# Performance work log

Hardware: AMD Instinct MI355X
Metric: run time of the kernel (lower is better)

Reference implementation:

```python
import jax, jax.numpy as jnp
import numpy as np

B, N, D = 1, 2048, 2048
H, DH, DR, MP = 16, 128, 64, 4
LOCAL = H * DH // MP  # per-shard qkv width
ATTN_MASK_VALUE = -1e10
LN_EPS = 1e-5


def setup_inputs() -> dict:
    key = jax.random.key(0)
    ks = jax.random.split(key, 5)
    s = 0.02
    return {
        "x": jax.random.normal(ks[0], (B, N, D), jnp.float32),
        "ln_scale": jnp.ones((D,), jnp.float32),
        "ln_offset": jnp.zeros((D,), jnp.float32),
        "w_qkv": jax.random.normal(ks[1], (D, 3 * H * DH), jnp.float32) * s,
        "w_attn_out": jax.random.normal(ks[2], (H * DH, D), jnp.float32) * s,
        "w_ff_in": jax.random.normal(ks[3], (D, 4 * D), jnp.float32) * s,
        "b_ff_in": jnp.zeros((4 * D,), jnp.float32),
        "w_ff_out": jax.random.normal(ks[4], (4 * D, D), jnp.float32) * s,
        "b_ff_out": jnp.zeros((D,), jnp.float32),
    }


def _rotate_every_two(x):
    # (..., d) -> interleaved (-x2, x1) pairs, GPT-J style
    x1 = x[..., ::2]
    x2 = x[..., 1::2]
    return jnp.stack((-x2, x1), axis=-1).reshape(x.shape)


def _fixed_pos_embedding(n, dim):
    inv_freq = 1.0 / (10000.0 ** (np.arange(0, dim, 2, dtype=np.float32) / dim))
    ang = np.einsum("i,j->ij", np.arange(n, dtype=np.float32), inv_freq)  # [n, dim/2]
    return jnp.asarray(np.sin(ang), jnp.float32), jnp.asarray(np.cos(ang), jnp.float32)


def _apply_rotary(x, sin, cos):
    # x: [b, n, h, d_rot]; sin/cos: [n, d_rot/2] repeated pairwise -> [1, n, 1, d_rot]
    sin = jnp.repeat(sin, 2, axis=-1)[None, :, None, :]
    cos = jnp.repeat(cos, 2, axis=-1)[None, :, None, :]
    return x * cos + _rotate_every_two(x) * sin


def reference(x, ln_scale, ln_offset, w_qkv, w_attn_out, w_ff_in, b_ff_in, w_ff_out, b_ff_out):
    # ---- LayerNorm (shared input to parallel attn + FFN) ----
    mu = jnp.mean(x, axis=-1, keepdims=True)
    var = jnp.var(x, axis=-1, keepdims=True)
    h = (x - mu) * jax.lax.rsqrt(var + LN_EPS) * ln_scale + ln_offset

    # ---- Causal self-attention with partial rotary ----
    qkv = (h @ w_qkv).reshape(B, N, MP, 3 * LOCAL)  # mp-sharded layout
    q, v, k = jnp.split(qkv, [LOCAL, 2 * LOCAL], axis=-1)
    heads = lambda t: t.reshape(B, N, H, DH)  # shard_heads: [b,n,mp,local] -> [b,n,h,dh]
    q, v, k = heads(q), heads(v), heads(k)

    sin, cos = _fixed_pos_embedding(N, DR)
    q = jnp.concatenate([_apply_rotary(q[..., :DR], sin, cos), q[..., DR:]], axis=-1)
    k = jnp.concatenate([_apply_rotary(k[..., :DR], sin, cos), k[..., DR:]], axis=-1)

    attn_scale = np.float32(np.sqrt(DH))
    logits = jnp.einsum("bihd,bjhd->bhij", q, k) / attn_scale
    causal_mask = jnp.triu(jnp.ones((N, N), dtype=bool), 1)
    logits = jnp.where(causal_mask, ATTN_MASK_VALUE, logits)
    attn_w = jax.nn.softmax(logits, axis=-1)
    attn_vec = jnp.einsum("bhij,bjhd->bihd", attn_w, v).reshape(B, N, H * DH)
    attn_out = attn_vec @ w_attn_out

    # ---- FFN (parallel branch, same LN input) ----
    ff_out = jax.nn.gelu(h @ w_ff_in + b_ff_in) @ w_ff_out + b_ff_out

    return attn_out + ff_out
```

## Files before the change

### kernel.cpp

```cpp
#include <hip/hip_runtime.h>
#include <hip/hip_bf16.h>

using bf16_t = __hip_bfloat16;
typedef __attribute__((ext_vector_type(8))) __bf16 bfrag;
typedef __attribute__((ext_vector_type(4))) float f32x4;

#define MFMA16(a, b, c) __builtin_amdgcn_mfma_f32_16x16x32_bf16((a), (b), (c), 0, 0, 0)

__device__ __forceinline__ void gload_lds16(const void* g, void* l) {
  __builtin_amdgcn_global_load_lds((const __attribute__((address_space(1))) void*)g,
                                   (__attribute__((address_space(3))) void*)l, 16, 0, 0);
}

__device__ __forceinline__ float bf2f(unsigned u) { return __uint_as_float(u << 16); }

__global__ __launch_bounds__(256) void transpose_cvt4(
    const float* __restrict__ in0, bf16_t* __restrict__ out0,
    const float* __restrict__ in1, bf16_t* __restrict__ out1,
    const float* __restrict__ in2, bf16_t* __restrict__ out2,
    const float* __restrict__ in3, bf16_t* __restrict__ out3) {
  __shared__ float t[64][65];
  int b = blockIdx.x;
  const float* in; bf16_t* out; int K, N, nx;
  if (b < 3072)      { in = in0; out = out0; K = 2048; N = 6144; nx = 96; }
  else if (b < 4096) { in = in1; out = out1; K = 2048; N = 2048; nx = 32; b -= 3072; }
  else if (b < 8192) { in = in2; out = out2; K = 2048; N = 8192; nx = 128; b -= 4096; }
  else               { in = in3; out = out3; K = 8192; N = 2048; nx = 32; b -= 8192; }
  const int n0 = (b % nx) * 64, k0 = (b / nx) * 64;
  const int tx = threadIdx.x & 15, ty = threadIdx.x >> 4;
#pragma unroll
  for (int i = 0; i < 4; ++i) {
    float4 v = *(const float4*)&in[(size_t)(k0 + i * 16 + ty) * N + n0 + tx * 4];
    t[i * 16 + ty][tx * 4 + 0] = v.x; t[i * 16 + ty][tx * 4 + 1] = v.y;
    t[i * 16 + ty][tx * 4 + 2] = v.z; t[i * 16 + ty][tx * 4 + 3] = v.w;
  }
  __syncthreads();
#pragma unroll
  for (int i = 0; i < 4; ++i) {
    const int n = i * 16 + ty;
    bf16_t w[4];
#pragma unroll
    for (int j = 0; j < 4; ++j) w[j] = bf16_t(t[tx * 4 + j][n]);
    *(uint2*)&out[(size_t)(n0 + n) * K + k0 + tx * 4] = *(const uint2*)w;
  }
}

__global__ __launch_bounds__(256) void ln_kernel(const float* __restrict__ x,
    const float* __restrict__ sc, const float* __restrict__ of, bf16_t* __restrict__ h) {
  __shared__ float red[8];
  const int n = blockIdx.x, tid = threadIdx.x;
  const float* xr = x + (size_t)n * 2048;
  float4 a = ((const float4*)xr)[tid * 2];
  float4 b = ((const float4*)xr)[tid * 2 + 1];
  float s = a.x + a.y + a.z + a.w + b.x + b.y + b.z + b.w;
  float q = a.x * a.x + a.y * a.y + a.z * a.z + a.w * a.w +
            b.x * b.x + b.y * b.y + b.z * b.z + b.w * b.w;
#pragma unroll
  for (int m = 32; m; m >>= 1) { s += __shfl_xor(s, m); q += __shfl_xor(q, m); }
  if ((tid & 63) == 0) { red[(tid >> 6) * 2] = s; red[(tid >> 6) * 2 + 1] = q; }
  __syncthreads();
  s = red[0] + red[2] + red[4] + red[6];
  q = red[1] + red[3] + red[5] + red[7];
  const float mu = s * (1.f / 2048.f);
  const float inv = rsqrtf(q * (1.f / 2048.f) - mu * mu + 1e-5f);
  const int base = tid * 8;
  float v[8] = {a.x, a.y, a.z, a.w, b.x, b.y, b.z, b.w};
  bf16_t* hr = h + (size_t)n * 2048 + base;
#pragma unroll
  for (int j = 0; j < 8; ++j) hr[j] = bf16_t((v[j] - mu) * inv * sc[base + j] + of[base + j]);
}

template <int EPI>
__global__ __launch_bounds__(512, 2) void gemm8p(
    const bf16_t* __restrict__ A, int lda, const bf16_t* __restrict__ BT, int ldb,
    const float* __restrict__ bias, float* __restrict__ Cf, bf16_t* __restrict__ Cb,
    int M, int N, int K, size_t splitStride) {
  extern __shared__ __align__(16) char lds[];
  const int tid = threadIdx.x, wid = tid >> 6, lane = tid & 63;
  const int lc = lane & 15, lg = lane >> 4;
  const int bm = blockIdx.y * 256, bn = blockIdx.x * 256;
  const int wr = wid >> 2, wc = wid & 3;
  const int NT = K >> 6, niter = NT >> 1;
  const int srow = tid >> 3;
  const int scol = (((tid & 7) ^ ((tid >> 3) & 7)) << 3);
  const bf16_t* Abase = A + (size_t)blockIdx.z * K + (size_t)(bm + srow) * lda + scol;
  const bf16_t* Bbase = BT + (size_t)blockIdx.z * K + (size_t)(bn + srow) * ldb + scol;
  auto SA = [&](int T, int h) {
    char* dst = lds + (T & 1) * 32768 + h * 16384 + wid * 1024;
    const bf16_t* src = Abase + (size_t)(h * 128) * lda + T * 64;
    gload_lds16(src, dst); gload_lds16(src + (size_t)64 * lda, dst + 8192);
  };
  auto SB = [&](int T, int h) {
    char* dst = lds + 65536 + (T & 1) * 32768 + h * 16384 + wid * 1024;
    const bf16_t* src = Bbase + (size_t)(h * 128) * ldb + T * 64;
    gload_lds16(src, dst); gload_lds16(src + (size_t)64 * ldb, dst + 8192);
  };
#define FRA(d, row, kk) (*(const bfrag*)(lds + (d) * 32768 + wr * 16384 + (row) * 128 + \
    ((((kk) * 4 + lg) ^ ((row) & 7)) << 4)))
#define FRB(d, row, kk) (*(const bfrag*)(lds + 65536 + (d) * 32768 + (wc >> 1) * 16384 + \
    (row) * 128 + ((((kk) * 4 + lg) ^ ((row) & 7)) << 4)))
#define PHASE_SYNC() do { __builtin_amdgcn_s_barrier(); \
    asm volatile("s_waitcnt lgkmcnt(0)" ::: "memory"); \
    __builtin_amdgcn_sched_barrier(0); __builtin_amdgcn_s_setprio(1); } while (0)
#define PHASE_END() do { __builtin_amdgcn_s_setprio(0); __builtin_amdgcn_s_barrier(); } while (0)
#define PHASE_END_VM(lastf) do { __builtin_amdgcn_s_setprio(0); \
    if (lastf) asm volatile("s_waitcnt vmcnt(0)" ::: "memory"); \
    else       asm volatile("s_waitcnt vmcnt(4)" ::: "memory"); \
    __builtin_amdgcn_s_barrier(); } while (0)

  SB(0, 0); SB(0, 1); SA(0, 0); SA(0, 1); SB(1, 0); SB(1, 1);
  asm volatile("s_waitcnt vmcnt(4)" ::: "memory");
  __builtin_amdgcn_s_barrier();

  f32x4 acc[8][4] = {};
  const int brl = (wc & 1) * 64 + lc;

  for (int k = 0; k < niter; ++k) {
    const int T1 = 2 * k + 1, T2 = 2 * k + 2, T3 = 2 * k + 3;
    const bool last = (k == niter - 1);
    bfrag aq[4][2], b01[2][2], b23[2][2];
#pragma unroll 1
    for (int d = 0; d < 2; ++d) {
#pragma unroll
      for (int m = 0; m < 4; ++m)
#pragma unroll
        for (int kk = 0; kk < 2; ++kk) aq[m][kk] = FRA(d, m * 16 + lc, kk);
#pragma unroll
      for (int n = 0; n < 2; ++n)
#pragma unroll
        for (int kk = 0; kk < 2; ++kk) b01[n][kk] = FRB(d, brl + n * 16, kk);
      if (d == 0) SA(T1, 0); else if (!last) SA(T2, 0);
      PHASE_SYNC();
#pragma unroll
      for (int kk = 0; kk < 2; ++kk)
#pragma unroll
        for (int m = 0; m < 4; ++m) {
          acc[m][0] = MFMA16(aq[m][kk], b01[0][kk], acc[m][0]);
          acc[m][1] = MFMA16(aq[m][kk], b01[1][kk], acc[m][1]);
        }
      PHASE_END();
#pragma unroll
      for (int n = 0; n < 2; ++n)
#pragma unroll
        for (int kk = 0; kk < 2; ++kk) b23[n][kk] = FRB(d, brl + (n + 2) * 16, kk);
      if (d == 0) SA(T1, 1); else if (!last) SA(T2, 1);
      PHASE_SYNC();
#pragma unroll
      for (int kk = 0; kk < 2; ++kk)
#pragma unroll
        for (int m = 0; m < 4; ++m) {
          acc[m][2] = MFMA16(aq[m][kk], b23[0][kk], acc[m][2]);
          acc[m][3] = MFMA16(aq[m][kk], b23[1][kk], acc[m][3]);
        }
      PHASE_END();
#pragma unroll
      for (int m = 0; m < 4; ++m)
#pragma unroll
        for (int kk = 0; kk < 2; ++kk) aq[m][kk] = FRA(d, (m + 4) * 16 + lc, kk);
      if (!last) { if (d == 0) SB(T2, 0); else SB(T3, 0); }
      PHASE_SYNC();
#pragma unroll
      for (int kk = 0; kk < 2; ++kk)
#pragma unroll
        for (int m = 0; m < 4; ++m) {
          acc[4 + m][2] = MFMA16(aq[m][kk], b23[0][kk], acc[4 + m][2]);
          acc[4 + m][3] = MFMA16(aq[m][kk], b23[1][kk], acc[4 + m][3]);
        }
      PHASE_END();
      if (!last) { if (d == 0) SB(T2, 1); else SB(T3, 1); }
      PHASE_SYNC();
#pragma unroll
      for (int kk = 0; kk < 2; ++kk)
#pragma unroll
        for (int m = 0; m < 4; ++m) {
          acc[4 + m][0] = MFMA16(aq[m][kk], b01[0][kk], acc[4 + m][0]);
          acc[4 + m][1] = MFMA16(aq[m][kk], b01[1][kk], acc[4 + m][1]);
        }
      PHASE_END_VM(last);
    }
  }
#undef FRA
#undef FRB
#undef PHASE_SYNC
#undef PHASE_END
#undef PHASE_END_VM
  char* W = lds + wid * 16384;
  if (EPI & 8) {
    bf16_t* Wb = (bf16_t*)W;
    bf16_t* Cbz = Cb + (size_t)blockIdx.z * splitStride;
#pragma unroll
    for (int mc = 0; mc < 2; ++mc) {
#pragma unroll
      for (int m4 = 0; m4 < 4; ++m4) {
#pragma unroll
        for (int n = 0; n < 4; ++n) {
          const int col = bn + wc * 64 + n * 16 + lc;
          float bv = (EPI & 1) ? bias[col] : 0.f;
#pragma unroll
          for (int i = 0; i < 4; ++i) {
            float v = acc[mc * 4 + m4][n][i];
            if (EPI & 1) v += bv;
            if (EPI & 2) v = 0.5f * v * (1.f + tanhf(0.7978845608028654f * (v + 0.044715f * v * v * v)));
            Wb[(m4 * 16 + lg * 4 + i) * 72 + n * 16 + lc] = bf16_t(v);
          }
        }
      }
      asm volatile("s_waitcnt lgkmcnt(0)" ::: "memory");
      __builtin_amdgcn_sched_barrier(0);
#pragma unroll
      for (int p = 0; p < 8; ++p) {
        const int rl = p * 8 + (lane >> 3), j = lane & 7;
        uint4 v = *(const uint4*)&Wb[rl * 72 + j * 8];
        const int grow = bm + wr * 128 + mc * 64 + rl;
        const int gcol = bn + wc * 64 + j * 8;
        *(uint4*)&Cbz[(size_t)grow * N + gcol] = v;
      }
      asm volatile("s_waitcnt lgkmcnt(0)" ::: "memory");
      __builtin_amdgcn_sched_barrier(0);
    }
  } else {
    float* Wf = (float*)W;
    float* Cfz = Cf + (size_t)blockIdx.z * splitStride;
#pragma unroll
    for (int mc = 0; mc < 4; ++mc) {
#pragma unroll
      for (int m2 = 0; m2 < 2; ++m2) {
#pragma unroll
        for (int n = 0; n < 4; ++n) {
          const int col = bn + wc * 64 + n * 16 + lc;
          float bv = (EPI & 1) ? bias[col] : 0.f;
#pragma unroll
          for (int i = 0; i < 4; ++i) {
            float v = acc[mc * 2 + m2][n][i];
            if (EPI & 1) v += bv;
            if (EPI & 2) v = 0.5f * v * (1.f + tanhf(0.7978845608028654f * (v + 0.044715f * v * v * v)));
            Wf[(m2 * 16 + lg * 4 + i) * 72 + n * 16 + lc] = v;
          }
        }
      }
      asm volatile("s_waitcnt lgkmcnt(0)" ::: "memory");
      __builtin_amdgcn_sched_barrier(0);
#pragma unroll
      for (int p = 0; p < 8; ++p) {
        const int rl = p * 4 + (lane >> 4), j = lane & 15;
        float4 v = *(const float4*)&Wf[rl * 72 + j * 4];
        const int grow = bm + wr * 128 + mc * 32 + rl;
        const int gcol = bn + wc * 64 + j * 4;
        *(float4*)&Cfz[(size_t)grow * N + gcol] = v;
      }
      asm volatile("s_waitcnt lgkmcnt(0)" ::: "memory");
      __builtin_amdgcn_sched_barrier(0);
    }
  }
}

template <int NP, bool ADDIN, bool BIAS>
__global__ __launch_bounds__(256) void reduceP(const float* __restrict__ p0,
    const float* __restrict__ p1, const float* __restrict__ p2,
    const float* __restrict__ p3, const float* __restrict__ bias,
    float* __restrict__ out, int total, int colmask) {
  const int i = (blockIdx.x * 256 + threadIdx.x) * 4;
  if (i >= total) return;
  float4 v = *(const float4*)(p0 + i);
  float4 w = *(const float4*)(p1 + i);
  v.x += w.x; v.y += w.y; v.z += w.z; v.w += w.w;
  if (NP == 4) {
    float4 u = *(const float4*)(p2 + i);
    float4 z = *(const float4*)(p3 + i);
    v.x += u.x + z.x; v.y += u.y + z.y; v.z += u.z + z.z; v.w += u.w + z.w;
  }
  if (BIAS) {
    float4 b = *(const float4*)(bias + (i & colmask));
    v.x += b.x; v.y += b.y; v.z += b.z; v.w += b.w;
  }
  if (ADDIN) {
    float4 o = *(const float4*)(out + i);
    v.x += o.x; v.y += o.y; v.z += o.z; v.w += o.w;
  }
  *(float4*)(out + i) = v;
}

__global__ __launch_bounds__(256) void reduce4b(const bf16_t* __restrict__ p0,
    const bf16_t* __restrict__ p1, const bf16_t* __restrict__ p2,
    const bf16_t* __restrict__ p3, float* __restrict__ out, int total) {
  const int i = (blockIdx.x * 256 + threadIdx.x) * 8;
  if (i >= total) return;
  uint4 a0 = *(const uint4*)(p0 + i);
  uint4 a1 = *(const uint4*)(p1 + i);
  uint4 a2 = *(const uint4*)(p2 + i);
  uint4 a3 = *(const uint4*)(p3 + i);
  const unsigned* u0 = (const unsigned*)&a0;
  const unsigned* u1 = (const unsigned*)&a1;
  const unsigned* u2 = (const unsigned*)&a2;
  const unsigned* u3 = (const unsigned*)&a3;
  float r[8];
#pragma unroll
  for (int j = 0; j < 8; ++j) {
    const int w = j >> 1, sh = (j & 1) * 16;
    r[j] = bf2f((u0[w] >> sh) & 0xffffu) + bf2f((u1[w] >> sh) & 0xffffu) +
           bf2f((u2[w] >> sh) & 0xffffu) + bf2f((u3[w] >> sh) & 0xffffu);
  }
  *(float4*)(out + i) = make_float4(r[0], r[1], r[2], r[3]);
  *(float4*)(out + i + 4) = make_float4(r[4], r[5], r[6], r[7]);
}

__global__ __launch_bounds__(128) void rope_kernel(const bf16_t* __restrict__ qkv,
    bf16_t* __restrict__ qh, bf16_t* __restrict__ kh, bf16_t* __restrict__ vT) {
  const int n = blockIdx.x, hh = blockIdx.y;
  const int d = threadIdx.x;
  const int mp = hh >> 2, hi = hh & 3;
  const bf16_t* row = qkv + (size_t)n * 6144 + mp * 1536 + hi * 128;
  float q = __bfloat162float(row[d]);
  float k = __bfloat162float(row[1024 + d]);
  if (d < 64) {
    const float ang = (float)n * powf(10000.f, -(float)(d & ~1) / 64.f);
    const float sn = sinf(ang), cs = cosf(ang);
    const float qp = __shfl_xor(q, 1), kp = __shfl_xor(k, 1);
    if (d & 1) { q = q * cs + qp * sn; k = k * cs + kp * sn; }
    else       { q = q * cs - qp * sn; k = k * cs - kp * sn; }
  }
  qh[((size_t)hh * 2048 + n) * 128 + d] = bf16_t(q * 0.08838834764831845f);
  kh[((size_t)hh * 2048 + n) * 128 + d] = bf16_t(k);
  vT[((size_t)hh * 128 + d) * 2048 + n] = row[512 + d];
}

__global__ __launch_bounds__(256) void attn_kernel(const bf16_t* __restrict__ qh,
    const bf16_t* __restrict__ kh, const bf16_t* __restrict__ vT,
    bf16_t* __restrict__ Op, float2* __restrict__ ml) {
  __shared__ alignas(16) char Kbuf[2][16384];
  __shared__ alignas(16) char Vbuf[2][16384];
  __shared__ alignas(16) bf16_t Ps[4][16 * 72];
  const int p = blockIdx.x, h = blockIdx.y, z = blockIdx.z;
  const int tid = threadIdx.x, wid = tid >> 6, lane = tid & 63;
  const int lc = lane & 15, lg = lane >> 4;
  const int krow = wid * 4 + (lane >> 4);
  const int vrow = wid * 8 + (lane >> 3);

  auto stage = [&](int kv0, int d) {
#pragma unroll
    for (int i = 0; i < 4; ++i) {
      const int kr = i * 16 + krow;
      const int kch = (lane & 15) ^ (kr & 15);
      gload_lds16(kh + ((size_t)h * 2048 + kv0 + kr) * 128 + kch * 8,
                  Kbuf[d] + i * 4096 + wid * 1024);
      const int vr = i * 32 + vrow;
      const int vch = (lane & 7) ^ (vr & 7);
      gload_lds16(vT + ((size_t)h * 128 + vr) * 2048 + kv0 + vch * 8,
                  Vbuf[d] + i * 4096 + wid * 1024);
    }
  };
#define FRK(d, row, ch) (*(const bfrag*)(Kbuf[d] + (row) * 256 + (((ch) ^ ((row) & 15)) << 4)))
#define FRV(d, row, ch) (*(const bfrag*)(Vbuf[d] + (row) * 128 + (((ch) ^ ((row) & 7)) << 4)))

#pragma unroll 1
  for (int half = 0; half < 2; ++half) {
    const int qt = half ? (31 - p) : p;
    const int nkv = qt + 1;
    const int lo = (z * nkv) / 3, hi = ((z + 1) * nkv) / 3;
    const int nj = hi - lo;
    const int qr = qt * 64 + wid * 16;
    const bf16_t* Qb = qh + ((size_t)h * 2048 + qr) * 128;
    bfrag qf[4];
#pragma unroll
    for (int ks = 0; ks < 4; ++ks)
      qf[ks] = *(const bfrag*)&Qb[lc * 128 + ks * 32 + lg * 8];
    f32x4 O[8] = {};
    float mr[4] = {-1e30f, -1e30f, -1e30f, -1e30f};
    float lsum[4] = {0.f, 0.f, 0.f, 0.f};

    if (nj > 0) {
      stage(lo * 64, 0);
      asm volatile("s_waitcnt vmcnt(0)" ::: "memory");
      __builtin_amdgcn_s_barrier();
    }
#pragma unroll 1
    for (int j = 0; j < nj; ++j) {
      const int kt = lo + j, d = j & 1;
      const int kv0 = kt * 64;
      if (j + 1 < nj) stage(kv0 + 64, d ^ 1);
      f32x4 s[4];
#pragma unroll
      for (int c = 0; c < 4; ++c) {
        f32x4 a = {};
#pragma unroll
        for (int ks = 0; ks < 4; ++ks) {
          bfrag kf = FRK(d, c * 16 + lc, ks * 4 + lg);
          a = MFMA16(qf[ks], kf, a);
        }
        s[c] = a;
      }
      if (kt == qt) {
#pragma unroll
        for (int c = 0; c < 4; ++c)
#pragma unroll
          for (int i = 0; i < 4; ++i)
            if (kv0 + c * 16 + lc > qr + lg * 4 + i) s[c][i] = -1e10f;
      }
      float pm[4];
#pragma unroll
      for (int i = 0; i < 4; ++i)
        pm[i] = fmaxf(fmaxf(s[0][i], s[1][i]), fmaxf(s[2][i], s[3][i]));
#pragma unroll
      for (int m = 1; m < 16; m <<= 1)
#pragma unroll
        for (int i = 0; i < 4; ++i) pm[i] = fmaxf(pm[i], __shfl_xor(pm[i], m));
      bool small = true;
#pragma unroll
      for (int i = 0; i < 4; ++i) small = small && (pm[i] <= mr[i] + 8.f);
      const bool skip = __all(small);
      float al[4], rs[4];
#pragma unroll
      for (int i = 0; i < 4; ++i) {
        const float mn = skip ? mr[i] : fmaxf(mr[i], pm[i]);
        al[i] = __expf(mr[i] - mn);
        mr[i] = mn;
        rs[i] = 0.f;
      }
#pragma unroll
      for (int c = 0; c < 4; ++c)
#pragma unroll
        for (int i = 0; i < 4; ++i) {
          const float pv = __expf(s[c][i] - mr[i]);
          s[c][i] = pv; rs[i] += pv;
        }
#pragma unroll
      for (int m = 1; m < 16; m <<= 1)
#pragma unroll
        for (int i = 0; i < 4; ++i) rs[i] += __shfl_xor(rs[i], m);
#pragma unroll
      for (int i = 0; i < 4; ++i) lsum[i] = lsum[i] * al[i] + rs[i];
      if (!skip) {
#pragma unroll
        for (int n = 0; n < 8; ++n)
#pragma unroll
          for (int i = 0; i < 4; ++i) O[n][i] *= al[i];
      }
#pragma unroll
      for (int c = 0; c < 4; ++c)
#pragma unroll
        for (int i = 0; i < 4; ++i)
          Ps[wid][(lg * 4 + i) * 72 + c * 16 + lc] = bf16_t(s[c][i]);
#pragma unroll
      for (int k2 = 0; k2 < 2; ++k2) {
        bfrag pf = *(const bfrag*)((const char*)&Ps[wid][0] + lc * 144 + k2 * 64 + lg * 16);
#pragma unroll
        for (int n = 0; n < 8; ++n) {
          bfrag vf = FRV(d, n * 16 + lc, k2 * 4 + lg);
          O[n] = MFMA16(pf, vf, O[n]);
        }
      }
      if (j + 1 < nj) asm volatile("s_waitcnt vmcnt(0)" ::: "memory");
      asm volatile("s_waitcnt lgkmcnt(0)" ::: "memory");
      __builtin_amdgcn_s_barrier();
    }
    const size_t rb = (size_t)(z * 16 + h) * 2048 + qr;
#pragma unroll
    for (int n = 0; n < 8; ++n)
#pragma unroll
      for (int i = 0; i < 4; ++i)
        Op[(rb + lg * 4 + i) * 128 + n * 16 + lc] = bf16_t(O[n][i]);
    if (lc == 0) {
#pragma unroll
      for (int i = 0; i < 4; ++i)
        ml[rb + lg * 4 + i] = make_float2(mr[i], lsum[i]);
    }
    __builtin_amdgcn_s_barrier();
  }
#undef FRK
#undef FRV
}

__global__ __launch_bounds__(256) void attn_combine(const bf16_t* __restrict__ Op,
    const float2* __restrict__ ml, bf16_t* __restrict__ av) {
  const int idx = blockIdx.x * 256 + threadIdx.x;
  const int t = idx & 15, hr = idx >> 4;
  const int ZS = 16 * 2048;
  const size_t ZO = (size_t)ZS * 128;
  const float2 m0 = ml[hr], m1 = ml[ZS + hr], m2 = ml[2 * ZS + hr];
  const float M = fmaxf(fmaxf(m0.x, m1.x), m2.x);
  const float w0 = __expf(m0.x - M), w1 = __expf(m1.x - M), w2 = __expf(m2.x - M);
  const float inv = 1.f / (w0 * m0.y + w1 * m1.y + w2 * m2.y);
  const bf16_t* p0 = Op + (size_t)hr * 128 + t * 8;
  uint4 a0 = *(const uint4*)p0;
  uint4 a1 = *(const uint4*)(p0 + ZO);
  uint4 a2 = *(const uint4*)(p0 + 2 * ZO);
  const unsigned* u0 = (const unsigned*)&a0;
  const unsigned* u1 = (const unsigned*)&a1;
  const unsigned* u2 = (const unsigned*)&a2;
  bf16_t ov[8];
#pragma unroll
  for (int j = 0; j < 8; ++j) {
    const int w = j >> 1, sh = (j & 1) * 16;
    ov[j] = bf16_t((w0 * bf2f((u0[w] >> sh) & 0xffffu) +
                    w1 * bf2f((u1[w] >> sh) & 0xffffu) +
                    w2 * bf2f((u2[w] >> sh) & 0xffffu)) * inv);
  }
  const int row = hr & 2047, hh = hr >> 11;
  *(uint4*)(av + (size_t)row * 2048 + hh * 128 + t * 8) = *(const uint4*)ov;
}

extern "C" void kernel_launch(void* const* d_in, const int* in_sizes, int n_in,
                              void* d_out, int out_size, void* d_ws, size_t ws_size,
                              hipStream_t stream) {
  const float* x        = (const float*)d_in[0];
  const float* ln_scale = (const float*)d_in[1];
  const float* ln_offset= (const float*)d_in[2];
  const float* w_qkv    = (const float*)d_in[3];
  const float* w_ao     = (const float*)d_in[4];
  const float* w_ff_in  = (const float*)d_in[5];
  const float* b_ff_in  = (const float*)d_in[6];
  const float* w_ff_out = (const float*)d_in[7];
  const float* b_ff_out = (const float*)d_in[8];
  float* out = (float*)d_out;

  char* ws = (char*)d_ws;
  bf16_t* wqkvT   = (bf16_t*)(ws);
  bf16_t* waoT    = (bf16_t*)(ws + 25165824);
  bf16_t* wffinT  = (bf16_t*)(ws + 33554432);
  bf16_t* wffoutT = (bf16_t*)(ws + 67108864);
  bf16_t* h       = (bf16_t*)(ws + 100663296);
  bf16_t* qhb     = (bf16_t*)(ws + 109051904);
  bf16_t* khb     = (bf16_t*)(ws + 117440512);
  bf16_t* vTb     = (bf16_t*)(ws + 125829120);
  bf16_t* avb     = (bf16_t*)(ws + 134217728);
  bf16_t* qkvb    = (bf16_t*)(ws + 142606336);
  bf16_t* ff1b    = qkvb;
  bf16_t* pab     = qkvb;
  float*  pf      = (float*)(ws);
  bf16_t* Opart   = (bf16_t*)(ws);
  float2* mlpart  = (float2*)(ws + 167772160);

  hipFuncSetAttribute((const void*)gemm8p<0>,  hipFuncAttributeMaxDynamicSharedMemorySize, 131072);
  hipFuncSetAttribute((const void*)gemm8p<8>,  hipFuncAttributeMaxDynamicSharedMemorySize, 131072);
  hipFuncSetAttribute((const void*)gemm8p<11>, hipFuncAttributeMaxDynamicSharedMemorySize, 131072);

  dim3 b256(256), b512(512);
  transpose_cvt4<<<dim3(12288), b256, 0, stream>>>(w_qkv, wqkvT, w_ao, waoT,
                                                   w_ff_in, wffinT, w_ff_out, wffoutT);
  ln_kernel<<<dim3(2048), b256, 0, stream>>>(x, ln_scale, ln_offset, h);

  gemm8p<8><<<dim3(24, 8, 1), b512, 131072, stream>>>(h, 2048, wqkvT, 2048,
      nullptr, nullptr, qkvb, 2048, 6144, 2048, 0);
  rope_kernel<<<dim3(2048, 16), dim3(128), 0, stream>>>(qkvb, qhb, khb, vTb);

  attn_kernel<<<dim3(16, 16, 3), b256, 0, stream>>>(qhb, khb, vTb, Opart, mlpart);
  attn_combine<<<dim3(2048), b256, 0, stream>>>(Opart, mlpart, avb);

  gemm8p<8><<<dim3(8, 8, 4), b512, 131072, stream>>>(avb, 2048, waoT, 2048,
      nullptr, nullptr, pab, 2048, 2048, 512, (size_t)2048 * 2048);
  reduce4b<<<dim3(2048), b256, 0, stream>>>(pab, pab + 4194304, pab + 2 * 4194304,
      pab + 3 * 4194304, out, 4194304);

  gemm8p<11><<<dim3(32, 8, 1), b512, 131072, stream>>>(h, 2048, wffinT, 2048,
      b_ff_in, nullptr, ff1b, 2048, 8192, 2048, 0);

  gemm8p<0><<<dim3(8, 8, 4), b512, 131072, stream>>>(ff1b, 8192, wffoutT, 8192,
      nullptr, pf, nullptr, 2048, 2048, 2048, (size_t)2048 * 2048);
  reduceP<4, true, true><<<dim3(4096), b256, 0, stream>>>(pf, pf + 4194304,
      pf + 2 * 4194304, pf + 3 * 4194304, b_ff_out, out, 4194304, 2047);
}
```

Measured before the change: 412.5 us.

## Fuse LayerNorm into prep kernel and merge split-K reductions into one bf16 pass

LayerNorm now runs as extra blocks of the weight transpose/convert kernel, saving one launch. The FFN-out split-K GEMM now writes bf16 partials instead of fp32. A single final kernel sums the attention-out and FFN-out partials and adds the bias, replacing two reduce kernels and the read-modify-write of the output. The FFN-in GEMM is moved before attention, and workspace buffers are remapped onto regions that are free by then. The aim is less HBM traffic and fewer launches, at the cost of bf16 rounding of the FFN partial sums.

```diff
diff --git a/kernel.cpp b/kernel.cpp
--- a/kernel.cpp
+++ b/kernel.cpp
@@ -14,13 +14,39 @@
 
 __device__ __forceinline__ float bf2f(unsigned u) { return __uint_as_float(u << 16); }
 
-__global__ __launch_bounds__(256) void transpose_cvt4(
+__global__ __launch_bounds__(256) void prep_kernel(
     const float* __restrict__ in0, bf16_t* __restrict__ out0,
     const float* __restrict__ in1, bf16_t* __restrict__ out1,
     const float* __restrict__ in2, bf16_t* __restrict__ out2,
-    const float* __restrict__ in3, bf16_t* __restrict__ out3) {
+    const float* __restrict__ in3, bf16_t* __restrict__ out3,
+    const float* __restrict__ x, const float* __restrict__ sc,
+    const float* __restrict__ of, bf16_t* __restrict__ hh) {
+  int b = blockIdx.x;
+  if (b >= 12288) {
+    __shared__ float red[8];
+    const int n = b - 12288, tid = threadIdx.x;
+    const float* xr = x + (size_t)n * 2048;
+    float4 a = ((const float4*)xr)[tid * 2];
+    float4 bb = ((const float4*)xr)[tid * 2 + 1];
+    float s = a.x + a.y + a.z + a.w + bb.x + bb.y + bb.z + bb.w;
+    float q = a.x * a.x + a.y * a.y + a.z * a.z + a.w * a.w +
+              bb.x * bb.x + bb.y * bb.y + bb.z * bb.z + bb.w * bb.w;
+#pragma unroll
+    for (int m = 32; m; m >>= 1) { s += __shfl_xor(s, m); q += __shfl_xor(q, m); }
+    if ((tid & 63) == 0) { red[(tid >> 6) * 2] = s; red[(tid >> 6) * 2 + 1] = q; }
+    __syncthreads();
+    s = red[0] + red[2] + red[4] + red[6];
+    q = red[1] + red[3] + red[5] + red[7];
+    const float mu = s * (1.f / 2048.f);
+    const float inv = rsqrtf(q * (1.f / 2048.f) - mu * mu + 1e-5f);
+    const int base = tid * 8;
+    float v[8] = {a.x, a.y, a.z, a.w, bb.x, bb.y, bb.z, bb.w};
+    bf16_t* hr = hh + (size_t)n * 2048 + base;
+#pragma unroll
+    for (int j = 0; j < 8; ++j) hr[j] = bf16_t((v[j] - mu) * inv * sc[base + j] + of[base + j]);
+    return;
+  }
   __shared__ float t[64][65];
-  int b = blockIdx.x;
   const float* in; bf16_t* out; int K, N, nx;
   if (b < 3072)      { in = in0; out = out0; K = 2048; N = 6144; nx = 96; }
   else if (b < 4096) { in = in1; out = out1; K = 2048; N = 2048; nx = 32; b -= 3072; }
@@ -43,31 +69,6 @@
     for (int j = 0; j < 4; ++j) w[j] = bf16_t(t[tx * 4 + j][n]);
     *(uint2*)&out[(size_t)(n0 + n) * K + k0 + tx * 4] = *(const uint2*)w;
   }
-}
-
-__global__ __launch_bounds__(256) void ln_kernel(const float* __restrict__ x,
-    const float* __restrict__ sc, const float* __restrict__ of, bf16_t* __restrict__ h) {
-  __shared__ float red[8];
-  const int n = blockIdx.x, tid = threadIdx.x;
-  const float* xr = x + (size_t)n * 2048;
-  float4 a = ((const float4*)xr)[tid * 2];
-  float4 b = ((const float4*)xr)[tid * 2 + 1];
-  float s = a.x + a.y + a.z + a.w + b.x + b.y + b.z + b.w;
-  float q = a.x * a.x + a.y * a.y + a.z * a.z + a.w * a.w +
-            b.x * b.x + b.y * b.y + b.z * b.z + b.w * b.w;
-#pragma unroll
-  for (int m = 32; m; m >>= 1) { s += __shfl_xor(s, m); q += __shfl_xor(q, m); }
-  if ((tid & 63) == 0) { red[(tid >> 6) * 2] = s; red[(tid >> 6) * 2 + 1] = q; }
-  __syncthreads();
-  s = red[0] + red[2] + red[4] + red[6];
-  q = red[1] + red[3] + red[5] + red[7];
-  const float mu = s * (1.f / 2048.f);
-  const float inv = rsqrtf(q * (1.f / 2048.f) - mu * mu + 1e-5f);
-  const int base = tid * 8;
-  float v[8] = {a.x, a.y, a.z, a.w, b.x, b.y, b.z, b.w};
-  bf16_t* hr = h + (size_t)n * 2048 + base;
-#pragma unroll
-  for (int j = 0; j < 8; ++j) hr[j] = bf16_t((v[j] - mu) * inv * sc[base + j] + of[base + j]);
 }
 
 template <int EPI>
@@ -254,52 +255,30 @@
   }
 }
 
-template <int NP, bool ADDIN, bool BIAS>
-__global__ __launch_bounds__(256) void reduceP(const float* __restrict__ p0,
-    const float* __restrict__ p1, const float* __restrict__ p2,
-    const float* __restrict__ p3, const float* __restrict__ bias,
-    float* __restrict__ out, int total, int colmask) {
-  const int i = (blockIdx.x * 256 + threadIdx.x) * 4;
-  if (i >= total) return;
-  float4 v = *(const float4*)(p0 + i);
-  float4 w = *(const float4*)(p1 + i);
-  v.x += w.x; v.y += w.y; v.z += w.z; v.w += w.w;
-  if (NP == 4) {
-    float4 u = *(const float4*)(p2 + i);
-    float4 z = *(const float4*)(p3 + i);
-    v.x += u.x + z.x; v.y += u.y + z.y; v.z += u.z + z.z; v.w += u.w + z.w;
-  }
-  if (BIAS) {
-    float4 b = *(const float4*)(bias + (i & colmask));
-    v.x += b.x; v.y += b.y; v.z += b.z; v.w += b.w;
-  }
-  if (ADDIN) {
-    float4 o = *(const float4*)(out + i);
-    v.x += o.x; v.y += o.y; v.z += o.z; v.w += o.w;
-  }
-  *(float4*)(out + i) = v;
-}
-
-__global__ __launch_bounds__(256) void reduce4b(const bf16_t* __restrict__ p0,
-    const bf16_t* __restrict__ p1, const bf16_t* __restrict__ p2,
-    const bf16_t* __restrict__ p3, float* __restrict__ out, int total) {
+__global__ __launch_bounds__(256) void reduce_final(const bf16_t* __restrict__ pa,
+    const bf16_t* __restrict__ pfb, const float* __restrict__ bias,
+    float* __restrict__ out, int total) {
   const int i = (blockIdx.x * 256 + threadIdx.x) * 8;
   if (i >= total) return;
-  uint4 a0 = *(const uint4*)(p0 + i);
-  uint4 a1 = *(const uint4*)(p1 + i);
-  uint4 a2 = *(const uint4*)(p2 + i);
-  uint4 a3 = *(const uint4*)(p3 + i);
-  const unsigned* u0 = (const unsigned*)&a0;
-  const unsigned* u1 = (const unsigned*)&a1;
-  const unsigned* u2 = (const unsigned*)&a2;
-  const unsigned* u3 = (const unsigned*)&a3;
-  float r[8];
-#pragma unroll
-  for (int j = 0; j < 8; ++j) {
-    const int w = j >> 1, sh = (j & 1) * 16;
-    r[j] = bf2f((u0[w] >> sh) & 0xffffu) + bf2f((u1[w] >> sh) & 0xffffu) +
-           bf2f((u2[w] >> sh) & 0xffffu) + bf2f((u3[w] >> sh) & 0xffffu);
-  }
+  const size_t S = 4194304;
+  float r[8] = {};
+#pragma unroll
+  for (int z = 0; z < 4; ++z) {
+    uint4 a = *(const uint4*)(pa + z * S + i);
+    uint4 b = *(const uint4*)(pfb + z * S + i);
+    const unsigned* ua = (const unsigned*)&a;
+    const unsigned* ub = (const unsigned*)&b;
+#pragma unroll
+    for (int j = 0; j < 8; ++j) {
+      const int w = j >> 1, sh = (j & 1) * 16;
+      r[j] += bf2f((ua[w] >> sh) & 0xffffu) + bf2f((ub[w] >> sh) & 0xffffu);
+    }
+  }
+  const int cb = i & 2047;
+  float4 b0 = *(const float4*)(bias + cb);
+  float4 b1 = *(const float4*)(bias + cb + 4);
+  r[0] += b0.x; r[1] += b0.y; r[2] += b0.z; r[3] += b0.w;
+  r[4] += b1.x; r[5] += b1.y; r[6] += b1.z; r[7] += b1.w;
   *(float4*)(out + i) = make_float4(r[0], r[1], r[2], r[3]);
   *(float4*)(out + i + 4) = make_float4(r[4], r[5], r[6], r[7]);
 }
@@ -525,37 +504,33 @@
   bf16_t* avb     = (bf16_t*)(ws + 134217728);
   bf16_t* qkvb    = (bf16_t*)(ws + 142606336);
   bf16_t* ff1b    = qkvb;
-  bf16_t* pab     = qkvb;
-  float*  pf      = (float*)(ws);
   bf16_t* Opart   = (bf16_t*)(ws);
-  float2* mlpart  = (float2*)(ws + 167772160);
-
-  hipFuncSetAttribute((const void*)gemm8p<0>,  hipFuncAttributeMaxDynamicSharedMemorySize, 131072);
+  float2* mlpart  = (float2*)(ws + 100663296);
+  bf16_t* pab     = (bf16_t*)(ws + 33554432);
+  bf16_t* pfb     = (bf16_t*)(ws);
+
   hipFuncSetAttribute((const void*)gemm8p<8>,  hipFuncAttributeMaxDynamicSharedMemorySize, 131072);
   hipFuncSetAttribute((const void*)gemm8p<11>, hipFuncAttributeMaxDynamicSharedMemorySize, 131072);
 
   dim3 b256(256), b512(512);
-  transpose_cvt4<<<dim3(12288), b256, 0, stream>>>(w_qkv, wqkvT, w_ao, waoT,
-                                                   w_ff_in, wffinT, w_ff_out, wffoutT);
-  ln_kernel<<<dim3(2048), b256, 0, stream>>>(x, ln_scale, ln_offset, h);
+  prep_kernel<<<dim3(14336), b256, 0, stream>>>(w_qkv, wqkvT, w_ao, waoT,
+      w_ff_in, wffinT, w_ff_out, wffoutT, x, ln_scale, ln_offset, h);
 
   gemm8p<8><<<dim3(24, 8, 1), b512, 131072, stream>>>(h, 2048, wqkvT, 2048,
       nullptr, nullptr, qkvb, 2048, 6144, 2048, 0);
   rope_kernel<<<dim3(2048, 16), dim3(128), 0, stream>>>(qkvb, qhb, khb, vTb);
 
+  gemm8p<11><<<dim3(32, 8, 1), b512, 131072, stream>>>(h, 2048, wffinT, 2048,
+      b_ff_in, nullptr, ff1b, 2048, 8192, 2048, 0);
+
   attn_kernel<<<dim3(16, 16, 3), b256, 0, stream>>>(qhb, khb, vTb, Opart, mlpart);
   attn_combine<<<dim3(2048), b256, 0, stream>>>(Opart, mlpart, avb);
 
   gemm8p<8><<<dim3(8, 8, 4), b512, 131072, stream>>>(avb, 2048, waoT, 2048,
       nullptr, nullptr, pab, 2048, 2048, 512, (size_t)2048 * 2048);
-  reduce4b<<<dim3(2048), b256, 0, stream>>>(pab, pab + 4194304, pab + 2 * 4194304,
-      pab + 3 * 4194304, out, 4194304);
-
-  gemm8p<11><<<dim3(32, 8, 1), b512, 131072, stream>>>(h, 2048, wffinT, 2048,
-      b_ff_in, nullptr, ff1b, 2048, 8192, 2048, 0);
-
-  gemm8p<0><<<dim3(8, 8, 4), b512, 131072, stream>>>(ff1b, 8192, wffoutT, 8192,
-      nullptr, pf, nullptr, 2048, 2048, 2048, (size_t)2048 * 2048);
-  reduceP<4, true, true><<<dim3(4096), b256, 0, stream>>>(pf, pf + 4194304,
-      pf + 2 * 4194304, pf + 3 * 4194304, b_ff_out, out, 4194304, 2047);
-}
+
+  gemm8p<8><<<dim3(8, 8, 4), b512, 131072, stream>>>(ff1b, 8192, wffoutT, 8192,
+      nullptr, nullptr, pfb, 2048, 2048, 2048, (size_t)2048 * 2048);
+
+  reduce_final<<<dim3(2048), b256, 0, stream>>>(pab, pfb, b_ff_out, out, 4194304);
+}
```

New measurement: 393.4 us. 4.6% less time.
